# Kernel optimization log

Hardware: AMD Instinct MI355X
Metric: run time of the kernel (lower is better)

The kernel has to match this reference:

```python
import jax, jax.numpy as jnp
import numpy as np

B, L, D = 8, 256, 256
HN = 8            # head_num
HS = D // HN      # head_size
NEG = jnp.float32(-2.0**32 + 1)


def _split_heads(x):
    # torch.cat(torch.split(x, HS, dim=2), dim=0): head-major -> [HN*B, L, HS]
    b, l, _ = x.shape
    return x.reshape(b, l, HN, HS).transpose(2, 0, 1, 3).reshape(HN * b, l, HS)


def _split_heads_tm(t):
    # [B, L, L, D] -> [HN*B, L, L, HS], head-major on axis 0
    b, l, _, _ = t.shape
    return t.reshape(b, l, l, HN, HS).transpose(3, 0, 1, 2, 4).reshape(HN * b, l, l, HS)


def setup_inputs() -> dict:
    key = jax.random.key(0)
    ks = jax.random.split(key, 12)
    inp = {
        "queries": jax.random.normal(ks[0], (B, L, D), jnp.float32),
        "keys": jax.random.normal(ks[1], (B, L, D), jnp.float32),
        "time_mask": jnp.zeros((B, L, L), jnp.bool_),
        "attn_mask": jnp.triu(jnp.ones((L, L), jnp.bool_), k=1),  # causal: mask future
        "time_matrix_K": jax.random.normal(ks[2], (B, L, L, D), jnp.float32) * 0.05,
        "time_matrix_V": jax.random.normal(ks[3], (B, L, L, D), jnp.float32) * 0.05,
        "abs_pos_K": jax.random.normal(ks[4], (B, L, D), jnp.float32),
        "abs_pos_V": jax.random.normal(ks[5], (B, L, D), jnp.float32),
        "Q_w": jax.random.normal(ks[6], (D, D), jnp.float32) / np.sqrt(D),
        "Q_b": jnp.zeros((D,), jnp.float32),
        "K_w": jax.random.normal(ks[7], (D, D), jnp.float32) / np.sqrt(D),
        "K_b": jnp.zeros((D,), jnp.float32),
        "V_w": jax.random.normal(ks[8], (D, D), jnp.float32) / np.sqrt(D),
        "V_b": jnp.zeros((D,), jnp.float32),
    }
    return inp


def reference(queries, keys, time_mask, attn_mask, time_matrix_K, time_matrix_V,
              abs_pos_K, abs_pos_V, Q_w, Q_b, K_w, K_b, V_w, V_b):
    Q = queries @ Q_w.T + Q_b
    K = keys @ K_w.T + K_b
    V = keys @ V_w.T + V_b

    Q_, K_, V_ = _split_heads(Q), _split_heads(K), _split_heads(V)          # [HN*B, L, HS]
    tK_, tV_ = _split_heads_tm(time_matrix_K), _split_heads_tm(time_matrix_V)  # [HN*B, L, L, HS]
    pK_, pV_ = _split_heads(abs_pos_K), _split_heads(abs_pos_V)

    attn = jnp.einsum('bid,bjd->bij', Q_, K_)
    attn += jnp.einsum('bid,bjd->bij', Q_, pK_)
    attn += jnp.einsum('blij,blj->bli', tK_, Q_)
    attn = attn / jnp.sqrt(jnp.float32(HS))

    # NOTE: original expands time_mask batch-major (repeat_interleave) while
    # attn is head-major; reproduced faithfully.
    tm = jnp.repeat(time_mask, HN, axis=0)                # [B*HN, L, L]
    am = jnp.broadcast_to(attn_mask[None], attn.shape)
    attn = jnp.where(tm | am, NEG, attn)
    attn = jax.nn.softmax(attn, axis=-1)

    out = attn @ V_
    out += attn @ pV_
    out += jnp.einsum('bij,bijh->bih', attn, tV_)         # [HN*B, L, HS]

    # torch.cat(torch.split(out, B, dim=0), dim=2)
    out = out.reshape(HN, B, L, HS).transpose(1, 2, 0, 3).reshape(B, L, D)
    return out
```

## Files before the change

kernel.cpp:

```cpp
#include <hip/hip_runtime.h>
#include <hip/hip_bf16.h>
#include <math.h>

#define Bq 8
#define Lq 256
#define Dq 256
#define HNq 8
#define HSq 32

#define PROJ_ROWS 8

__global__ __launch_bounds__(256) void proj_kernel(
    const float* __restrict__ queries, const float* __restrict__ keys,
    const float* __restrict__ apK, const float* __restrict__ apV,
    const float* __restrict__ Qw, const float* __restrict__ Qb,
    const float* __restrict__ Kw, const float* __restrict__ Kb,
    const float* __restrict__ Vw, const float* __restrict__ Vb,
    float* __restrict__ Q, float* __restrict__ KpK, float* __restrict__ VpV)
{
    __shared__ float inq[PROJ_ROWS][Dq];
    __shared__ float ink[PROJ_ROWS][Dq];
    const int r0 = blockIdx.x * PROJ_ROWS;
    const int tid = threadIdx.x;

    for (int idx = tid; idx < PROJ_ROWS * Dq; idx += 256) {
        int r = idx >> 8, c = idx & 255;
        inq[r][c] = queries[(size_t)(r0 + r) * Dq + c];
        ink[r][c] = keys[(size_t)(r0 + r) * Dq + c];
    }
    __syncthreads();

    const int d = tid;
    float aq[PROJ_ROWS], ak[PROJ_ROWS], av[PROJ_ROWS];
#pragma unroll
    for (int r = 0; r < PROJ_ROWS; ++r) { aq[r] = 0.f; ak[r] = 0.f; av[r] = 0.f; }

    const float4* qwr = (const float4*)(Qw + (size_t)d * Dq);
    const float4* kwr = (const float4*)(Kw + (size_t)d * Dq);
    const float4* vwr = (const float4*)(Vw + (size_t)d * Dq);

    for (int k4 = 0; k4 < Dq / 4; ++k4) {
        float4 wq = qwr[k4], wk = kwr[k4], wv = vwr[k4];
        int k = k4 * 4;
#pragma unroll
        for (int r = 0; r < PROJ_ROWS; ++r) {
            float i0 = inq[r][k], i1 = inq[r][k + 1], i2 = inq[r][k + 2], i3 = inq[r][k + 3];
            aq[r] += i0 * wq.x + i1 * wq.y + i2 * wq.z + i3 * wq.w;
            float j0 = ink[r][k], j1 = ink[r][k + 1], j2 = ink[r][k + 2], j3 = ink[r][k + 3];
            ak[r] += j0 * wk.x + j1 * wk.y + j2 * wk.z + j3 * wk.w;
            av[r] += j0 * wv.x + j1 * wv.y + j2 * wv.z + j3 * wv.w;
        }
    }

    const float qb = Qb[d], kb = Kb[d], vb = Vb[d];
#pragma unroll
    for (int r = 0; r < PROJ_ROWS; ++r) {
        size_t o = (size_t)(r0 + r) * Dq + d;
        Q[o]   = aq[r] + qb;
        KpK[o] = ak[r] + kb + apK[o];
        VpV[o] = av[r] + vb + apV[o];
    }
}

__global__ __launch_bounds__(256) void attn_kernel(
    const float* __restrict__ Q, const float* __restrict__ KpK,
    const float* __restrict__ VpV,
    const float* __restrict__ tmK, const float* __restrict__ tmV,
    float* __restrict__ out)
{
    const int i  = blockIdx.x;
    const int hb = blockIdx.y;
    const int h  = hb >> 3;
    const int b  = hb & 7;
    const int tid = threadIdx.x;
    const int l8 = tid & 7;
    const int g  = tid >> 3;

    __shared__ float qs[HSq];
    __shared__ float sb[Lq];
    __shared__ float red[4];
    __shared__ float po[32][HSq];

    if (tid < HSq) qs[tid] = Q[((size_t)(b * Lq + i)) * Dq + h * HSq + tid];
    __syncthreads();

    const float4 q4 = ((const float4*)qs)[l8];

    const size_t tkRow = (((size_t)b * Lq + i) * Lq) * Dq + h * HSq;
    const size_t kvRow = ((size_t)b * Lq) * Dq + h * HSq;
    const int c4 = l8 * 4;

#pragma unroll
    for (int p = 0; p < 8; ++p) {
        const int j = p * 32 + g;
        if (j <= i) {
            float4 tk = *(const float4*)(tmK + tkRow + (size_t)j * Dq + c4);
            float4 kp = *(const float4*)(KpK + kvRow + (size_t)j * Dq + c4);
            float v = q4.x * (tk.x + kp.x) + q4.y * (tk.y + kp.y)
                    + q4.z * (tk.z + kp.z) + q4.w * (tk.w + kp.w);
            v += __shfl_xor(v, 1);
            v += __shfl_xor(v, 2);
            v += __shfl_xor(v, 4);
            if (l8 == 0) sb[j] = v * 0.17677669529663687f;
        }
    }
    __syncthreads();

    float sc = (tid <= i) ? sb[tid] : -3.0e38f;
    float m = sc;
#pragma unroll
    for (int off = 32; off >= 1; off >>= 1) m = fmaxf(m, __shfl_xor(m, off));
    if ((tid & 63) == 0) red[tid >> 6] = m;
    __syncthreads();
    m = fmaxf(fmaxf(red[0], red[1]), fmaxf(red[2], red[3]));

    float pr = (tid <= i) ? __expf(sc - m) : 0.f;
    float sum = pr;
#pragma unroll
    for (int off = 32; off >= 1; off >>= 1) sum += __shfl_xor(sum, off);
    __syncthreads();
    if ((tid & 63) == 0) red[tid >> 6] = sum;
    __syncthreads();
    sum = red[0] + red[1] + red[2] + red[3];
    sb[tid] = pr / sum;
    __syncthreads();

    const size_t tvRow = (((size_t)b * Lq + i) * Lq) * Dq + h * HSq;
    float4 acc = make_float4(0.f, 0.f, 0.f, 0.f);
#pragma unroll
    for (int p = 0; p < 8; ++p) {
        const int j = p * 32 + g;
        if (j <= i) {
            float pp = sb[j];
            float4 tv = *(const float4*)(tmV + tvRow + (size_t)j * Dq + c4);
            float4 vv = *(const float4*)(VpV + kvRow + (size_t)j * Dq + c4);
            acc.x += pp * (tv.x + vv.x);
            acc.y += pp * (tv.y + vv.y);
            acc.z += pp * (tv.z + vv.z);
            acc.w += pp * (tv.w + vv.w);
        }
    }
    ((float4*)po[g])[l8] = acc;
    __syncthreads();

    if (tid < HSq) {
        float o = 0.f;
#pragma unroll
        for (int g2 = 0; g2 < 32; ++g2) o += po[g2][tid];
        out[((size_t)(b * Lq + i)) * Dq + h * HSq + tid] = o;
    }
}

extern "C" void kernel_launch(void* const* d_in, const int* in_sizes, int n_in,
                              void* d_out, int out_size, void* d_ws, size_t ws_size,
                              hipStream_t stream) {
    const float* queries = (const float*)d_in[0];
    const float* keys    = (const float*)d_in[1];
    const float* tmK = (const float*)d_in[4];
    const float* tmV = (const float*)d_in[5];
    const float* apK = (const float*)d_in[6];
    const float* apV = (const float*)d_in[7];
    const float* Qw  = (const float*)d_in[8];
    const float* Qb  = (const float*)d_in[9];
    const float* Kw  = (const float*)d_in[10];
    const float* Kb  = (const float*)d_in[11];
    const float* Vw  = (const float*)d_in[12];
    const float* Vb  = (const float*)d_in[13];
    float* out = (float*)d_out;

    const size_t n = (size_t)Bq * Lq * Dq;
    float* Q   = (float*)d_ws;
    float* KpK = Q + n;
    float* VpV = KpK + n;

    proj_kernel<<<dim3((Bq * Lq) / PROJ_ROWS), 256, 0, stream>>>(
        queries, keys, apK, apV, Qw, Qb, Kw, Kb, Vw, Vb, Q, KpK, VpV);

    attn_kernel<<<dim3(Lq, HNq * Bq), 256, 0, stream>>>(
        Q, KpK, VpV, tmK, tmV, out);
}
```

Measured before the change: 197.2 us.

## Process all heads per block with contiguous row loads and causal row pairing

The attention kernel now assigns one (batch, query row) to each block and handles all 8 heads at once. Each wavefront therefore reads a full contiguous 1 KB row of the time matrices instead of a 128-byte per-head slice, and those loads are marked nontemporal. Each block handles row x and row L-1-x so that causal work is balanced across blocks, and the softmax scale is folded into the Q projection. The grid shrinks to 1024 blocks with a sequential loop over two rows, which risks lower parallelism and less latency hiding.

```diff
diff --git a/kernel.cpp b/kernel.cpp
--- a/kernel.cpp
+++ b/kernel.cpp
@@ -1,5 +1,4 @@
 #include <hip/hip_runtime.h>
-#include <hip/hip_bf16.h>
 #include <math.h>
 
 #define Bq 8
@@ -7,6 +6,9 @@
 #define Dq 256
 #define HNq 8
 #define HSq 32
+#define PADq 260
+
+typedef float f4 __attribute__((ext_vector_type(4)));
 
 #define PROJ_ROWS 8
 
@@ -56,7 +58,7 @@
 #pragma unroll
     for (int r = 0; r < PROJ_ROWS; ++r) {
         size_t o = (size_t)(r0 + r) * Dq + d;
-        Q[o]   = aq[r] + qb;
+        Q[o]   = (aq[r] + qb) * 0.17677669529663687f;
         KpK[o] = ak[r] + kb + apK[o];
         VpV[o] = av[r] + vb + apV[o];
     }
@@ -68,86 +70,82 @@
     const float* __restrict__ tmK, const float* __restrict__ tmV,
     float* __restrict__ out)
 {
-    const int i  = blockIdx.x;
-    const int hb = blockIdx.y;
-    const int h  = hb >> 3;
-    const int b  = hb & 7;
+    const int x   = blockIdx.x;
+    const int b   = blockIdx.y;
     const int tid = threadIdx.x;
-    const int l8 = tid & 7;
-    const int g  = tid >> 3;
+    const int w    = tid >> 6;
+    const int lane = tid & 63;
+    const int h    = lane >> 3;
+    const int l8   = lane & 7;
+    const int c4   = h * HSq + l8 * 4;
 
-    __shared__ float qs[HSq];
-    __shared__ float sb[Lq];
-    __shared__ float red[4];
-    __shared__ float po[32][HSq];
+    __shared__ float qs[Dq];
+    __shared__ float sb[HNq * PADq];
+    __shared__ float po[4][Dq];
 
-    if (tid < HSq) qs[tid] = Q[((size_t)(b * Lq + i)) * Dq + h * HSq + tid];
-    __syncthreads();
+    const size_t rowB = (size_t)b * Lq * Dq;
 
-    const float4 q4 = ((const float4*)qs)[l8];
+    for (int hf = 0; hf < 2; ++hf) {
+        const int i = hf ? (Lq - 1 - x) : x;
 
-    const size_t tkRow = (((size_t)b * Lq + i) * Lq) * Dq + h * HSq;
-    const size_t kvRow = ((size_t)b * Lq) * Dq + h * HSq;
-    const int c4 = l8 * 4;
+        if (tid < 64)
+            ((f4*)qs)[tid] = ((const f4*)(Q + rowB + (size_t)i * Dq))[tid];
+        __syncthreads();
+        const f4 q4 = *(const f4*)(qs + c4);
 
+        const float* tkB = tmK + ((size_t)(b * Lq + i) * Lq) * Dq;
+        const float* tvB = tmV + ((size_t)(b * Lq + i) * Lq) * Dq;
+
+#pragma unroll 2
+        for (int j = w; j <= i; j += 4) {
+            f4 tk = __builtin_nontemporal_load((const f4*)(tkB + (size_t)j * Dq + c4));
+            f4 kp = *(const f4*)(KpK + rowB + (size_t)j * Dq + c4);
+            float s = q4[0] * (tk[0] + kp[0]) + q4[1] * (tk[1] + kp[1])
+                    + q4[2] * (tk[2] + kp[2]) + q4[3] * (tk[3] + kp[3]);
+            s += __shfl_xor(s, 1);
+            s += __shfl_xor(s, 2);
+            s += __shfl_xor(s, 4);
+            if (l8 == 0) sb[h * PADq + j] = s;
+        }
+        __syncthreads();
+
+        {
+            const int hh = tid >> 5, jl = tid & 31;
+            float vv[8];
+            float m = -3.0e38f;
 #pragma unroll
-    for (int p = 0; p < 8; ++p) {
-        const int j = p * 32 + g;
-        if (j <= i) {
-            float4 tk = *(const float4*)(tmK + tkRow + (size_t)j * Dq + c4);
-            float4 kp = *(const float4*)(KpK + kvRow + (size_t)j * Dq + c4);
-            float v = q4.x * (tk.x + kp.x) + q4.y * (tk.y + kp.y)
-                    + q4.z * (tk.z + kp.z) + q4.w * (tk.w + kp.w);
-            v += __shfl_xor(v, 1);
-            v += __shfl_xor(v, 2);
-            v += __shfl_xor(v, 4);
-            if (l8 == 0) sb[j] = v * 0.17677669529663687f;
+            for (int k = 0; k < 8; ++k) {
+                int j = jl + 32 * k;
+                vv[k] = (j <= i) ? sb[hh * PADq + j] : -3.0e38f;
+                m = fmaxf(m, vv[k]);
+            }
+#pragma unroll
+            for (int off = 16; off >= 1; off >>= 1) m = fmaxf(m, __shfl_xor(m, off));
+            float sum = 0.f;
+#pragma unroll
+            for (int k = 0; k < 8; ++k) { vv[k] = __expf(vv[k] - m); sum += vv[k]; }
+#pragma unroll
+            for (int off = 16; off >= 1; off >>= 1) sum += __shfl_xor(sum, off);
+            const float inv = 1.0f / sum;
+#pragma unroll
+            for (int k = 0; k < 8; ++k) sb[hh * PADq + jl + 32 * k] = vv[k] * inv;
         }
-    }
-    __syncthreads();
+        __syncthreads();
 
-    float sc = (tid <= i) ? sb[tid] : -3.0e38f;
-    float m = sc;
-#pragma unroll
-    for (int off = 32; off >= 1; off >>= 1) m = fmaxf(m, __shfl_xor(m, off));
-    if ((tid & 63) == 0) red[tid >> 6] = m;
-    __syncthreads();
-    m = fmaxf(fmaxf(red[0], red[1]), fmaxf(red[2], red[3]));
+        f4 acc = {0.f, 0.f, 0.f, 0.f};
+#pragma unroll 2
+        for (int j = w; j <= i; j += 4) {
+            float p = sb[h * PADq + j];
+            f4 tv = __builtin_nontemporal_load((const f4*)(tvB + (size_t)j * Dq + c4));
+            f4 vp = *(const f4*)(VpV + rowB + (size_t)j * Dq + c4);
+            acc += p * (tv + vp);
+        }
+        *(f4*)(po[w] + c4) = acc;
+        __syncthreads();
 
-    float pr = (tid <= i) ? __expf(sc - m) : 0.f;
-    float sum = pr;
-#pragma unroll
-    for (int off = 32; off >= 1; off >>= 1) sum += __shfl_xor(sum, off);
-    __syncthreads();
-    if ((tid & 63) == 0) red[tid >> 6] = sum;
-    __syncthreads();
-    sum = red[0] + red[1] + red[2] + red[3];
-    sb[tid] = pr / sum;
-    __syncthreads();
-
-    const size_t tvRow = (((size_t)b * Lq + i) * Lq) * Dq + h * HSq;
-    float4 acc = make_float4(0.f, 0.f, 0.f, 0.f);
-#pragma unroll
-    for (int p = 0; p < 8; ++p) {
-        const int j = p * 32 + g;
-        if (j <= i) {
-            float pp = sb[j];
-            float4 tv = *(const float4*)(tmV + tvRow + (size_t)j * Dq + c4);
-            float4 vv = *(const float4*)(VpV + kvRow + (size_t)j * Dq + c4);
-            acc.x += pp * (tv.x + vv.x);
-            acc.y += pp * (tv.y + vv.y);
-            acc.z += pp * (tv.z + vv.z);
-            acc.w += pp * (tv.w + vv.w);
-        }
-    }
-    ((float4*)po[g])[l8] = acc;
-    __syncthreads();
-
-    if (tid < HSq) {
-        float o = 0.f;
-#pragma unroll
-        for (int g2 = 0; g2 < 32; ++g2) o += po[g2][tid];
-        out[((size_t)(b * Lq + i)) * Dq + h * HSq + tid] = o;
+        out[rowB + (size_t)i * Dq + tid] =
+            po[0][tid] + po[1][tid] + po[2][tid] + po[3][tid];
+        __syncthreads();
     }
 }
 
@@ -176,6 +174,6 @@
     proj_kernel<<<dim3((Bq * Lq) / PROJ_ROWS), 256, 0, stream>>>(
         queries, keys, apK, apV, Qw, Qb, Kw, Kb, Vw, Vb, Q, KpK, VpV);
 
-    attn_kernel<<<dim3(Lq, HNq * Bq), 256, 0, stream>>>(
+    attn_kernel<<<dim3(Lq / 2, Bq), 256, 0, stream>>>(
         Q, KpK, VpV, tmK, tmV, out);
 }
```

Measured after the change: 174.1 us. 1.13x faster.
